# Performance work log

Measured on AMD Instinct MI355X. Metric: run time of the kernel, lower is better.

Reference implementation:

```python
import jax, jax.numpy as jnp
import numpy as np
import math

D_K = 64

def setup_inputs() -> dict:
    key = jax.random.key(0)
    ks = jax.random.split(key, 7)
    B, S, d = 8, 2048, D_K
    H = 4096
    Q = jax.random.normal(ks[0], (B, S, d), dtype=jnp.float32)
    K = jax.random.normal(ks[1], (B, S, d), dtype=jnp.float32)
    V = jax.random.normal(ks[2], (B, S, d), dtype=jnp.float32)
    # Linear params (stored as [in, out]); scaled like torch default init
    W1 = jax.random.normal(ks[3], (S, H), dtype=jnp.float32) / math.sqrt(S)
    b1 = jnp.zeros((H,), dtype=jnp.float32)
    W2 = jax.random.normal(ks[4], (H, S), dtype=jnp.float32) / math.sqrt(H)
    b2 = jnp.zeros((S,), dtype=jnp.float32)
    return {"Q": Q, "K": K, "V": V, "W1": W1, "b1": b1, "W2": W2, "b2": b2}

def reference(Q, K, V, W1, b1, W2, b2):
    # scores: [B, Sq, Sk]
    scores = jnp.einsum('bqd,bkd->bqk', Q, K) / jnp.sqrt(jnp.float32(D_K))
    # 2-layer MLP applied along the last (Sk) axis of the scores
    h = jax.nn.relu(jnp.einsum('bqk,kh->bqh', scores, W1) + b1)
    adjusted = jnp.einsum('bqh,hk->bqk', h, W2) + b2
    attn = jax.nn.softmax(adjusted, axis=-1)
    return jnp.einsum('bqk,bkd->bqd', attn, V)
```

## Files before the change

### kernel.cpp

```cpp
#include <hip/hip_runtime.h>
#include <hip/hip_bf16.h>
#include <stdint.h>

#define S 2048
#define D 64
#define H 4096
#define NB 8

typedef __bf16 bf16;
typedef __attribute__((ext_vector_type(8))) __bf16 bf16x8;
typedef __attribute__((ext_vector_type(4))) __bf16 bf16x4;
typedef __attribute__((ext_vector_type(4))) float f32x4;

__device__ __forceinline__ void dma16_raw(const bf16* g, uint32_t m0_bytes) {
  uint32_t m0s = __builtin_amdgcn_readfirstlane(m0_bytes);
  asm volatile("s_mov_b32 m0, %1\n\t"
               "global_load_lds_dwordx4 %0, off"
               :: "v"(g), "s"(m0s) : "memory");
}

__device__ __forceinline__ uint32_t lds_off_bytes(const void* p) {
  return (uint32_t)(uintptr_t)(__attribute__((address_space(3))) const void*)p;
}

__global__ __launch_bounds__(256) void transpose_cast(const float* __restrict__ W,
                                                      bf16* __restrict__ Wt,
                                                      int K, int N) {
  __shared__ float tile[64][65];
  int k0 = blockIdx.y * 64, n0 = blockIdx.x * 64;
  int c = threadIdx.x & 63;
  int r4 = threadIdx.x >> 6;
#pragma unroll
  for (int i = 0; i < 16; ++i) {
    int r = i * 4 + r4;
    tile[r][c] = W[(size_t)(k0 + r) * N + n0 + c];
  }
  __syncthreads();
#pragma unroll
  for (int i = 0; i < 16; ++i) {
    int r = i * 4 + r4;
    Wt[(size_t)(n0 + r) * K + k0 + c] = (bf16)tile[c][r];
  }
}

__global__ __launch_bounds__(256) void vt_cast(const float* __restrict__ V,
                                               bf16* __restrict__ Vt) {
  __shared__ float tile[64][65];
  int z = blockIdx.y;
  int s0 = blockIdx.x * 64;
  const float* Vb = V + (size_t)z * (S * D);
  bf16* Vtb = Vt + (size_t)z * (D * S);
  int c = threadIdx.x & 63;
  int r4 = threadIdx.x >> 6;
#pragma unroll
  for (int i = 0; i < 16; ++i) {
    int r = i * 4 + r4;
    tile[r][c] = Vb[(size_t)(s0 + r) * D + c];
  }
  __syncthreads();
#pragma unroll
  for (int i = 0; i < 16; ++i) {
    int r = i * 4 + r4;
    Vtb[(size_t)r * S + s0 + c] = (bf16)tile[c][r];
  }
}

__global__ __launch_bounds__(256) void cast_bf16(const float* __restrict__ x,
                                                 bf16* __restrict__ y) {
  int i = blockIdx.x * 256 + threadIdx.x;
  f32x4 v = ((const f32x4*)x)[i];
  bf16x4 o;
  o[0] = (bf16)v.x; o[1] = (bf16)v.y; o[2] = (bf16)v.z; o[3] = (bf16)v.w;
  ((bf16x4*)y)[i] = o;
}

template <int RELU, int OUTBF16>
__global__ __launch_bounds__(256, 2) void gemm_bt(const bf16* __restrict__ A,
                                                  const bf16* __restrict__ Bt,
                                                  const float* __restrict__ bias,
                                                  void* __restrict__ Cv,
                                                  float scale,
                                                  int M, int N, int K,
                                                  long strideA, long strideB,
                                                  long strideC) {
  __shared__ __align__(16) bf16 smem[24576];
  int tid = threadIdx.x;
  int lane = tid & 63;
  int w = tid >> 6;

  int m0 = blockIdx.y * 128, n0 = blockIdx.x * 256;
  const bf16* Ab = A + (size_t)blockIdx.z * strideA;
  const bf16* Btb = Bt + (size_t)blockIdx.z * strideB;

  int grow = tid >> 2;
  int gcol = (((lane & 3) ^ ((lane >> 3) & 3)) * 8);
  const bf16* gA0 = Ab + (size_t)(m0 + grow) * K + gcol;
  const bf16* gA1 = gA0 + (size_t)64 * K;
  const bf16* gB0 = Btb + (size_t)(n0 + grow) * K + gcol;
  const bf16* gB1 = gB0 + (size_t)64 * K;
  const bf16* gB2 = gB0 + (size_t)128 * K;
  const bf16* gB3 = gB0 + (size_t)192 * K;

  uint32_t ldsBase = lds_off_bytes(&smem[0]);
  uint32_t wb = (uint32_t)(w * 1024);
  uint32_t mA[2], mB[2];
  mA[0] = ldsBase + wb;          mA[1] = ldsBase + 8192 + wb;
  mB[0] = ldsBase + 16384 + wb;  mB[1] = ldsBase + 32768 + wb;

  int mw = (w & 1) * 64, nw = (w >> 1) * 128;
  int lr = lane & 15;
  int ck = lane >> 4;
  int swz = (ck ^ ((lr >> 1) & 3)) * 8;
  const bf16* paBase = smem + (size_t)(mw + lr) * 32 + swz;
  const bf16* pbBase = smem + 8192 + (size_t)(nw + lr) * 32 + swz;

  f32x4 zero = {0.f, 0.f, 0.f, 0.f};
  f32x4 acc[4][8];
#pragma unroll
  for (int mt = 0; mt < 4; ++mt)
#pragma unroll
    for (int nt = 0; nt < 8; ++nt) acc[mt][nt] = zero;

  const int niter = K / 32;

#define STAGE(buf, koff)                                 \
  do {                                                   \
    dma16_raw(gA0 + (koff), mA[buf]);                    \
    dma16_raw(gA1 + (koff), mA[buf] + 4096);             \
    dma16_raw(gB0 + (koff), mB[buf]);                    \
    dma16_raw(gB1 + (koff), mB[buf] + 4096);             \
    dma16_raw(gB2 + (koff), mB[buf] + 8192);             \
    dma16_raw(gB3 + (koff), mB[buf] + 12288);            \
  } while (0)

  STAGE(0, 0);
  STAGE(1, 32);

  for (int it = 0; it < niter; ++it) {
    int buf = it & 1;
    asm volatile("s_waitcnt vmcnt(6)\n\ts_barrier" ::: "memory");
    const bf16* pa = paBase + buf * 4096;
    const bf16* pb = pbBase + buf * 8192;
    bf16x8 af[4], bfr[8];
#pragma unroll
    for (int mt = 0; mt < 4; ++mt) af[mt] = *(const bf16x8*)(pa + mt * (16 * 32));
#pragma unroll
    for (int nt = 0; nt < 8; ++nt) bfr[nt] = *(const bf16x8*)(pb + nt * (16 * 32));
    asm volatile("s_waitcnt lgkmcnt(0)\n\ts_barrier" ::: "memory");
    int kpre = it + 2 < niter ? (it + 2) * 32 : (niter - 1) * 32;
    STAGE(buf, kpre);
#pragma unroll
    for (int mt = 0; mt < 4; ++mt)
#pragma unroll
      for (int nt = 0; nt < 8; ++nt)
        acc[mt][nt] = __builtin_amdgcn_mfma_f32_16x16x32_bf16(af[mt], bfr[nt],
                                                              acc[mt][nt], 0, 0, 0);
  }
#undef STAGE
  asm volatile("s_waitcnt vmcnt(0)" ::: "memory");

  int mbase = m0 + mw + (lane >> 4) * 4;
  int nbase = n0 + nw + (lane & 15);
#pragma unroll
  for (int mt = 0; mt < 4; ++mt) {
#pragma unroll
    for (int nt = 0; nt < 8; ++nt) {
      int n = nbase + nt * 16;
      float bv = bias ? bias[n] : 0.f;
#pragma unroll
      for (int reg = 0; reg < 4; ++reg) {
        int m = mbase + mt * 16 + reg;
        float v = acc[mt][nt][reg] * scale + bv;
        if (RELU) v = fmaxf(v, 0.f);
        if (OUTBF16) {
          bf16* C = (bf16*)Cv + (size_t)blockIdx.z * strideC;
          C[(size_t)m * N + n] = (bf16)v;
        } else {
          float* C = (float*)Cv + (size_t)blockIdx.z * strideC;
          C[(size_t)m * N + n] = v;
        }
      }
    }
  }
}

template <int RELU, int OUTBF16>
__global__ __launch_bounds__(512, 2) void gemm256(const bf16* __restrict__ A,
                                                  const bf16* __restrict__ Bt,
                                                  const float* __restrict__ bias,
                                                  void* __restrict__ Cv,
                                                  float scale,
                                                  int M, int N, int K,
                                                  long strideA, long strideB,
                                                  long strideC) {
  __shared__ __align__(16) bf16 smem[65536];
  const char* smc = (const char*)&smem[0];

  int tid = threadIdx.x;
  int lane = tid & 63;
  int w = tid >> 6;
  int wm = w >> 2, wn = w & 3;

  unsigned gx = gridDim.x;
  unsigned nwg = gx * gridDim.y;
  unsigned flat = blockIdx.y * gx + blockIdx.x;
  unsigned q = nwg >> 3, r = nwg & 7, xcd = flat & 7, idx = flat >> 3;
  unsigned wg = (xcd < r ? xcd * (q + 1) : r * (q + 1) + (xcd - r) * q) + idx;
  int n0 = (int)(wg % gx) * 256;
  int m0 = (int)(wg / gx) * 256;

  const bf16* Ab = A + (size_t)blockIdx.z * strideA;
  const bf16* Btb = Bt + (size_t)blockIdx.z * strideB;

  int trow = tid >> 3;
  int tg = (tid & 7) ^ (trow & 7);
  const bf16* pgA = Ab + (size_t)(m0 + trow) * K + tg * 8;
  const bf16* pgB = Btb + (size_t)(n0 + trow) * K + tg * 8;
  const size_t s64K = (size_t)K * 64;

  uint32_t ldsBase = lds_off_bytes(&smem[0]);
  uint32_t mb = ldsBase + (uint32_t)(w * 1024);

  int j = lane >> 4, b2 = (lane >> 2) & 1;
  uint32_t rbA0 = (uint32_t)(wm * 8192 + (lane & 15) * 128 +
                             ((j ^ (lane & 3)) * 16) + b2 * 64);
  uint32_t rbA1 = rbA0 ^ 64u;
  uint32_t rbB0 = (uint32_t)(65536 + wn * 4096 + (lane & 15) * 128 +
                             ((j ^ (lane & 3)) * 16) + b2 * 64);
  uint32_t rbB1 = rbB0 ^ 64u;

  f32x4 acc[8][4];
#pragma unroll
  for (int a = 0; a < 8; ++a)
#pragma unroll
    for (int b = 0; b < 2 * 2; ++b) acc[a][b] = (f32x4){0.f, 0.f, 0.f, 0.f};

  bf16x8 af[4][2];
  bf16x8 bf0[2][2];
  bf16x8 bf1[2][2];

#define STG_A(PI, HH, LL, KC) \
  dma16_raw(pgA + (size_t)(2 * (HH) + (LL)) * s64K + (KC), \
            mb + (PI) * 32768 + (HH) * 16384 + (LL) * 8192)
#define STG_B(PI, HH, LL, KC) \
  dma16_raw(pgB + (size_t)(2 * (HH) + (LL)) * s64K + (KC), \
            mb + 65536 + (PI) * 32768 + (HH) * 16384 + (LL) * 8192)
#define STAGE_AH(PI, HH, KC) do { STG_A(PI, HH, 0, KC); STG_A(PI, HH, 1, KC); } while (0)
#define STAGE_BH(PI, HH, KC) do { STG_B(PI, HH, 0, KC); STG_B(PI, HH, 1, KC); } while (0)

#define RDA(PI, QA)                                                            \
  do {                                                                        \
    _Pragma("unroll") for (int mt = 0; mt < 4; ++mt) {                        \
      af[mt][0] = *(const bf16x8*)(smc + rbA0 + ((PI) * 32768 + (QA) * 16384 + mt * 2048)); \
      af[mt][1] = *(const bf16x8*)(smc + rbA1 + ((PI) * 32768 + (QA) * 16384 + mt * 2048)); \
    }                                                                         \
  } while (0)
#define RDB(PI, QB, BF)                                                        \
  do {                                                                        \
    _Pragma("unroll") for (int nt = 0; nt < 2; ++nt) {                        \
      BF[nt][0] = *(const bf16x8*)(smc + rbB0 + ((PI) * 32768 + (QB) * 16384 + nt * 2048)); \
      BF[nt][1] = *(const bf16x8*)(smc + rbB1 + ((PI) * 32768 + (QB) * 16384 + nt * 2048)); \
    }                                                                         \
  } while (0)

#define MFMA_Q(QA, QB, BF)                                                     \
  do {                                                                        \
    __builtin_amdgcn_s_setprio(1);                                            \
    _Pragma("unroll") for (int mt = 0; mt < 4; ++mt)                          \
      _Pragma("unroll") for (int nt = 0; nt < 2; ++nt) {                      \
        f32x4 c = acc[(QA) * 4 + mt][(QB) * 2 + nt];                          \
        c = __builtin_amdgcn_mfma_f32_16x16x32_bf16(af[mt][0], BF[nt][0], c, 0, 0, 0); \
        c = __builtin_amdgcn_mfma_f32_16x16x32_bf16(af[mt][1], BF[nt][1], c, 0, 0, 0); \
        acc[(QA) * 4 + mt][(QB) * 2 + nt] = c;                                \
      }                                                                       \
    __builtin_amdgcn_s_setprio(0);                                            \
  } while (0)

#define BAR() asm volatile("s_barrier" ::: "memory")
#define VMC4() asm volatile("s_waitcnt vmcnt(4)" ::: "memory")

#define TILE(PI, KC1, KC2)            \
  do {                                \
    RDA(PI, 0);                       \
    RDB(PI, 0, bf0);                  \
    STAGE_AH((PI) ^ 1, 1, KC1);       \
    BAR();                            \
    MFMA_Q(0, 0, bf0);                \
    RDB(PI, 1, bf1);                  \
    STAGE_BH((PI) ^ 1, 0, KC1);       \
    BAR();                            \
    MFMA_Q(0, 1, bf1);                \
    RDA(PI, 1);                       \
    STAGE_AH(PI, 0, KC2);             \
    BAR();                            \
    MFMA_Q(1, 1, bf1);                \
    STAGE_BH(PI, 1, KC2);             \
    MFMA_Q(1, 0, bf0);                \
    VMC4();                           \
    BAR();                            \
  } while (0)

  STAGE_AH(0, 0, 0);
  STAGE_BH(0, 1, 0);
  STAGE_AH(0, 1, 0);
  STAGE_BH(0, 0, 0);
  STAGE_AH(1, 0, 64);
  STAGE_BH(1, 1, 64);
  asm volatile("s_waitcnt vmcnt(4)\n\ts_barrier" ::: "memory");

  const int NT = K / 64;
  for (int T = 0; T < NT; T += 2) {
    int c1 = (T + 1) * 64;
    int c2 = (T + 2 < NT ? T + 2 : NT - 1) * 64;
    int c3 = (T + 3 < NT ? T + 3 : NT - 1) * 64;
    TILE(0, c1, c2);
    TILE(1, c2, c3);
  }
#undef TILE
#undef VMC4
#undef BAR
#undef MFMA_Q
#undef RDB
#undef RDA
#undef STAGE_BH
#undef STAGE_AH
#undef STG_B
#undef STG_A

  asm volatile("s_waitcnt vmcnt(0)" ::: "memory");

  int rowb = m0 + wm * 64 + ((lane >> 4) << 2);
  int colb = n0 + wn * 32 + (lane & 15);
#pragma unroll
  for (int fn = 0; fn < 4; ++fn) {
    int n = colb + (fn >> 1) * 128 + (fn & 1) * 16;
    float bv = bias ? bias[n] : 0.f;
#pragma unroll
    for (int fm = 0; fm < 8; ++fm) {
      int mrow = rowb + (fm >> 2) * 128 + (fm & 3) * 16;
#pragma unroll
      for (int reg = 0; reg < 4; ++reg) {
        float v = acc[fm][fn][reg] * scale + bv;
        if (RELU) v = fmaxf(v, 0.f);
        int m = mrow + reg;
        if (OUTBF16) {
          bf16* C = (bf16*)Cv + (size_t)blockIdx.z * strideC;
          C[(size_t)m * N + n] = (bf16)v;
        } else {
          float* C = (float*)Cv + (size_t)blockIdx.z * strideC;
          C[(size_t)m * N + n] = v;
        }
      }
    }
  }
}

__global__ __launch_bounds__(256) void smav(const float* __restrict__ adj,
                                            const bf16* __restrict__ Vt,
                                            float* __restrict__ out,
                                            long adjStride) {
  int z = blockIdx.y;
  const float* adjb = adj + (size_t)z * adjStride;
  const bf16* Vtb = Vt + (size_t)z * (D * S);
  float* outb = out + (size_t)z * (S * D);
  int q0 = blockIdx.x * 16;
  __shared__ __align__(16) bf16 P[16 * 2048];
  __shared__ float rsum[16];
  int tid = threadIdx.x, w = tid >> 6, lane = tid & 63;
  char* Pc = (char*)&P[0];

#pragma unroll
  for (int i = 0; i < 4; ++i) {
    int r = w * 4 + i;
    const float* rowp = adjb + (size_t)(q0 + r) * S + lane * 4;
    f32x4 rv[8];
    float lm = -1e30f;
#pragma unroll
    for (int kk = 0; kk < 8; ++kk) {
      rv[kk] = *(const f32x4*)(rowp + kk * 256);
      lm = fmaxf(lm, fmaxf(fmaxf(rv[kk].x, rv[kk].y), fmaxf(rv[kk].z, rv[kk].w)));
    }
#pragma unroll
    for (int off = 32; off > 0; off >>= 1) lm = fmaxf(lm, __shfl_xor(lm, off));
    float s = 0.f;
    uint32_t wbase = (uint32_t)(r * 4096 + (lane & 1) * 8);
#pragma unroll
    for (int kk = 0; kk < 8; ++kk) {
      bf16x4 pb;
      pb[0] = (bf16)__expf(rv[kk].x - lm);
      pb[1] = (bf16)__expf(rv[kk].y - lm);
      pb[2] = (bf16)__expf(rv[kk].z - lm);
      pb[3] = (bf16)__expf(rv[kk].w - lm);
      s += (float)pb[0] + (float)pb[1] + (float)pb[2] + (float)pb[3];
      uint32_t g = (uint32_t)(lane >> 1) + (uint32_t)(kk * 32);
      uint32_t gs = g ^ (uint32_t)(r & 7);
      *(bf16x4*)(Pc + wbase + gs * 16) = pb;
    }
#pragma unroll
    for (int off = 32; off > 0; off >>= 1) s += __shfl_xor(s, off);
    if (lane == 0) rsum[r] = s;
  }
  __syncthreads();

  int dl = (w << 4) + (lane & 15);
  const bf16* vrow = Vtb + (size_t)dl * S + (lane >> 4) * 8;
  uint32_t rl = (uint32_t)(lane & 15);
  uint32_t abase = rl * 4096;
  uint32_t rx = rl & 7;
  f32x4 acc0 = {0.f, 0.f, 0.f, 0.f}, acc1 = {0.f, 0.f, 0.f, 0.f};
#pragma unroll 4
  for (int k0 = 0; k0 < S; k0 += 64) {
    uint32_t g0 = (uint32_t)(k0 >> 3) + (uint32_t)(lane >> 4);
    bf16x8 a0 = *(const bf16x8*)(Pc + abase + ((g0 ^ rx) * 16));
    bf16x8 b0 = *(const bf16x8*)(vrow + k0);
    acc0 = __builtin_amdgcn_mfma_f32_16x16x32_bf16(a0, b0, acc0, 0, 0, 0);
    uint32_t g1 = g0 + 4;
    bf16x8 a1 = *(const bf16x8*)(Pc + abase + ((g1 ^ rx) * 16));
    bf16x8 b1 = *(const bf16x8*)(vrow + k0 + 32);
    acc1 = __builtin_amdgcn_mfma_f32_16x16x32_bf16(a1, b1, acc1, 0, 0, 0);
  }
  f32x4 accs = acc0 + acc1;
#pragma unroll
  for (int reg = 0; reg < 4; ++reg) {
    int m = ((lane >> 4) << 2) + reg;
    outb[(size_t)(q0 + m) * D + dl] = accs[reg] / rsum[m];
  }
}

extern "C" void kernel_launch(void* const* d_in, const int* in_sizes, int n_in,
                              void* d_out, int out_size, void* d_ws, size_t ws_size,
                              hipStream_t stream) {
  const float* Q  = (const float*)d_in[0];
  const float* Km = (const float*)d_in[1];
  const float* V  = (const float*)d_in[2];
  const float* W1 = (const float*)d_in[3];
  const float* b1 = (const float*)d_in[4];
  const float* W2 = (const float*)d_in[5];
  const float* b2 = (const float*)d_in[6];
  float* out = (float*)d_out;
  char* ws = (char*)d_ws;

  bf16* W1t  = (bf16*)ws;
  bf16* W2t  = (bf16*)(ws + 16777216);
  bf16* Qb16 = (bf16*)(ws + 33554432);
  bf16* Kb16 = (bf16*)(ws + 35651584);

  transpose_cast<<<dim3(H / 64, S / 64), 256, 0, stream>>>(W1, W1t, S, H);
  transpose_cast<<<dim3(S / 64, H / 64), 256, 0, stream>>>(W2, W2t, H, S);
  cast_bf16<<<dim3(NB * S * D / 1024), 256, 0, stream>>>(Q, Qb16);
  cast_bf16<<<dim3(NB * S * D / 1024), 256, 0, stream>>>(Km, Kb16);

  int G = 1;
  if (ws_size >= 306184192ULL) G = 8;
  else if (ws_size >= 171966464ULL) G = 4;
  else if (ws_size >= 104857600ULL) G = 2;

  bf16* Sc   = (bf16*)(ws + 37748736);
  float* adj = (float*)(ws + 37748736);
  bf16* h    = (bf16*)(ws + 37748736 + (size_t)G * 16777216);
  bf16* Vt   = h;

  for (int b0 = 0; b0 < NB; b0 += G) {
    gemm_bt<0, 1><<<dim3(S / 256, S / 128, G), 256, 0, stream>>>(
        Qb16 + (size_t)b0 * S * D, Kb16 + (size_t)b0 * S * D, nullptr, Sc,
        0.125f, S, S, D, (long)S * D, (long)S * D, (long)S * S);
    gemm256<1, 1><<<dim3(H / 256, S / 256, G), 512, 0, stream>>>(
        Sc, W1t, b1, h, 1.0f, S, H, S, (long)S * S, 0L, (long)S * H);
    gemm256<0, 0><<<dim3(S / 256, S / 256, G), 512, 0, stream>>>(
        h, W2t, b2, adj, 1.0f, S, S, H, (long)S * H, 0L, (long)S * S);
    vt_cast<<<dim3(S / 64, G), 256, 0, stream>>>(V + (size_t)b0 * S * D, Vt);
    smav<<<dim3(S / 16, G), 256, 0, stream>>>(
        adj, Vt, out + (size_t)b0 * S * D, (long)S * S);
  }
}
```

Before: 659.7 us.

## Rotate GEMM main loop to prefetch next tile's first fragments during last MFMA quadrant

Restructures the software-pipelined GEMM main loop so the LDS reads of the next tile's first A/B fragments and the staging of the next A half are issued after the last MFMA quadrant of the current tile, with a prologue doing the first tile's reads. This is meant to hide LDS read latency behind MFMA work instead of stalling at the start of each tile. The reordering changes barrier placement and the staged K offsets, so it risks LDS hazards if the synchronisation is off.

```diff
diff --git a/kernel.cpp b/kernel.cpp
--- a/kernel.cpp
+++ b/kernel.cpp
@@ -279,25 +279,33 @@
 #define BAR() asm volatile("s_barrier" ::: "memory")
 #define VMC4() asm volatile("s_waitcnt vmcnt(4)" ::: "memory")
 
-#define TILE(PI, KC1, KC2)            \
-  do {                                \
-    RDA(PI, 0);                       \
-    RDB(PI, 0, bf0);                  \
-    STAGE_AH((PI) ^ 1, 1, KC1);       \
-    BAR();                            \
-    MFMA_Q(0, 0, bf0);                \
-    RDB(PI, 1, bf1);                  \
-    STAGE_BH((PI) ^ 1, 0, KC1);       \
-    BAR();                            \
-    MFMA_Q(0, 1, bf1);                \
-    RDA(PI, 1);                       \
-    STAGE_AH(PI, 0, KC2);             \
-    BAR();                            \
-    MFMA_Q(1, 1, bf1);                \
-    STAGE_BH(PI, 1, KC2);             \
-    MFMA_Q(1, 0, bf0);                \
-    VMC4();                           \
-    BAR();                            \
+#define TILE2(PI, TT)                                              \
+  do {                                                             \
+    int c1 = ((TT) + 1 < NT ? (TT) + 1 : NT - 1) * 64;             \
+    int c2 = ((TT) + 2 < NT ? (TT) + 2 : NT - 1) * 64;             \
+                                                           \
+    MFMA_Q(0, 0, bf0);                                             \
+    RDB(PI, 1, bf1);                                               \
+    STAGE_BH((PI) ^ 1, 0, c1);                                     \
+    BAR();                                                         \
+                                                           \
+    MFMA_Q(0, 1, bf1);                                             \
+    RDA(PI, 1);                                                    \
+    STAGE_AH(PI, 0, c2);                                           \
+    BAR();                                                         \
+      \
+    STAGE_BH(PI, 1, c2);                                           \
+    MFMA_Q(1, 1, bf1);                                             \
+    VMC4();                                                        \
+    BAR();                                                         \
+           \
+    MFMA_Q(1, 0, bf0);                                             \
+    if ((TT) + 1 < NT) {                                           \
+      RDA((PI) ^ 1, 0);                                            \
+      RDB((PI) ^ 1, 0, bf0);                                       \
+      STAGE_AH(PI, 1, c2);                                         \
+      BAR();                                                       \
+    }                                                              \
   } while (0)
 
   STAGE_AH(0, 0, 0);
@@ -309,14 +317,17 @@
   asm volatile("s_waitcnt vmcnt(4)\n\ts_barrier" ::: "memory");
 
   const int NT = K / 64;
+
+  RDA(0, 0);
+  RDB(0, 0, bf0);
+  STAGE_AH(1, 1, 64);
+  BAR();
+
   for (int T = 0; T < NT; T += 2) {
-    int c1 = (T + 1) * 64;
-    int c2 = (T + 2 < NT ? T + 2 : NT - 1) * 64;
-    int c3 = (T + 3 < NT ? T + 3 : NT - 1) * 64;
-    TILE(0, c1, c2);
-    TILE(1, c2, c3);
-  }
-#undef TILE
+    TILE2(0, T);
+    TILE2(1, T + 1);
+  }
+#undef TILE2
 #undef VMC4
 #undef BAR
 #undef MFMA_Q
```

New measurement: 644.2 us. 1.02x faster.
